# Kernel optimization log

Measured on AMD Instinct MI355X. Metric: run time of the kernel, lower is better.

The kernel has to match this reference:

```python
import jax, jax.numpy as jnp
import numpy as np

MODES, WIDTH, DEPTH, IN_F, OUT_F, HID = 8, 16, 3, 1, 1, 64


def setup_inputs() -> dict:
    key = jax.random.key(0)
    ks = jax.random.split(key, 12)
    B, H, W = 8, 512, 512
    scale = 1.0 / (WIDTH * WIDTH)
    inp = {
        'x': jax.random.normal(ks[0], (B, IN_F, H, W), dtype=jnp.float32),
        'fc0_w': jax.random.normal(ks[1], (IN_F, WIDTH), dtype=jnp.float32) * 0.5,
        'fc0_b': jax.random.normal(ks[2], (WIDTH,), dtype=jnp.float32) * 0.1,
        # complex spectral weights stored as real/imag parts, stacked over depth
        'spec_wr': jax.random.normal(ks[3], (DEPTH, WIDTH, WIDTH, MODES, MODES), dtype=jnp.float32) * scale,
        'spec_wi': jax.random.normal(ks[4], (DEPTH, WIDTH, WIDTH, MODES, MODES), dtype=jnp.float32) * scale,
        # 1x1 convs as [depth, out, in] matmuls + bias
        'conv_w': jax.random.normal(ks[5], (DEPTH, WIDTH, WIDTH), dtype=jnp.float32) * 0.25,
        'conv_b': jax.random.normal(ks[6], (DEPTH, WIDTH), dtype=jnp.float32) * 0.1,
        'fc1_w': jax.random.normal(ks[7], (WIDTH, HID), dtype=jnp.float32) * 0.25,
        'fc1_b': jax.random.normal(ks[8], (HID,), dtype=jnp.float32) * 0.1,
        'fc2_w': jax.random.normal(ks[9], (HID, OUT_F), dtype=jnp.float32) * 0.125,
        'fc2_b': jax.random.normal(ks[10], (OUT_F,), dtype=jnp.float32) * 0.1,
    }
    return inp


def _spectral_conv(x, w):
    # x: [B, Ci, H, W] real; w: [Ci, Co, m, m] complex
    B, C, H, W = x.shape
    m = w.shape[2]
    x_ft = jnp.fft.rfft2(x, norm='forward')  # [B, Ci, H, W//2+1]
    out_modes = jnp.einsum('bixy,ioxy->boxy', x_ft[:, :, :m, :m], w)
    out_ft = jnp.zeros((B, w.shape[1], H, W // 2 + 1), dtype=out_modes.dtype)
    out_ft = out_ft.at[:, :, :m, :m].set(out_modes)
    return jnp.fft.irfft2(out_ft, s=(H, W), norm='forward')


def reference(x, fc0_w, fc0_b, spec_wr, spec_wi, conv_w, conv_b, fc1_w, fc1_b, fc2_w, fc2_b):
    # lift: [B,C,H,W] -> channels-last linear -> [B,width,H,W]
    h = jnp.einsum('bchw,cd->bdhw', x, fc0_w) + fc0_b[None, :, None, None]
    for d in range(DEPTH):
        w_c = (spec_wr[d] + 1j * spec_wi[d]).astype(jnp.complex64)
        y = _spectral_conv(h, w_c)
        local = jnp.einsum('bchw,oc->bohw', h, conv_w[d]) + conv_b[d][None, :, None, None]
        h = y + local
    h = jnp.einsum('bchw,cd->bdhw', h, fc1_w) + fc1_b[None, :, None, None]
    h = jax.nn.relu(h)
    out = jnp.einsum('bchw,cd->bdhw', h, fc2_w) + fc2_b[None, :, None, None]
    return out
```

## Files before the change

### kernel.cpp

```cpp
#include <hip/hip_runtime.h>
#include <math.h>

#define NB 8
#define NH 512
#define NW 512
#define ANG512 0.01227184630308513f
#define SPEC_D 16384

#define DEV_SCOPE __HIP_MEMORY_SCOPE_AGENT

__global__ __launch_bounds__(256) void k_pre(const float* __restrict__ x,
                                             float* __restrict__ P,
                                             int* __restrict__ flags) {
    __shared__ float wred[8][16];
    const int tid = threadIdx.x;
    const int w = tid >> 6, lane = tid & 63;
    const int gid = blockIdx.x;
    const int b = gid >> 6, rg = gid & 63;

    if (gid == 0 && tid < 8)
        __hip_atomic_store(&flags[tid * 32], 0, __ATOMIC_RELAXED, DEV_SCOPE);

    #pragma unroll
    for (int rr = 0; rr < 2; ++rr) {
        const int row = rg * 8 + w + 4 * rr;
        const float* xr = x + ((size_t)(b * NH + row)) * NW;

        float p[16];
        #pragma unroll
        for (int j = 0; j < 16; ++j) p[j] = 0.f;

        #pragma unroll
        for (int j = 0; j < 4; ++j) {
            const int ww = lane + (j << 6);
            const float xa = xr[ww], xb = xr[ww + 256];
            const float a = xa + xb, d = xa - xb;
            float c1, s1;
            __sincosf(ANG512 * (float)ww, &s1, &c1);
            p[0] += a;
            p[1] = fmaf(d, c1, p[1]);
            p[9] = fmaf(-d, s1, p[9]);
            const float c2k = 2.f * c1;
            float ckm = 1.f, skm = 0.f, ck = c1, sk = s1;
            #pragma unroll
            for (int k = 2; k < 8; ++k) {
                const float cn = fmaf(c2k, ck, -ckm);
                const float sn = fmaf(c2k, sk, -skm);
                ckm = ck; skm = sk; ck = cn; sk = sn;
                const float v = (k & 1) ? d : a;
                p[k]     = fmaf(v, ck, p[k]);
                p[8 + k] = fmaf(-v, sk, p[8 + k]);
            }
        }
        #pragma unroll
        for (int m = 1; m < 64; m <<= 1) {
            #pragma unroll
            for (int j = 0; j < 16; ++j) p[j] += __shfl_xor(p[j], m);
        }
        if (lane < 16) wred[w + 4 * rr][lane] = p[lane];
    }
    __syncthreads();

    if (tid < 128) {
        const int kx = tid >> 4, q = tid & 15, qm = q & 7;
        float acc = 0.f;
        #pragma unroll
        for (int r = 0; r < 8; ++r) {
            const int row = rg * 8 + r;
            const int m = (kx * row) & 511;
            float cm, s2;
            __sincosf(ANG512 * (float)m, &s2, &cm);
            const float rre = wred[r][qm], rim = wred[r][8 + qm];
            acc += (q < 8) ? (rre * cm + rim * s2)
                           : (rim * cm - rre * s2);
        }
        P[((size_t)((b * 64 + rg) * 8 + kx)) * 16 + q] = acc;
    }
}

__device__ __forceinline__ void phaseC(
        const float* __restrict__ x, const float* __restrict__ AH,
        const float* __restrict__ gvec, const float* __restrict__ Kvec,
        const float* __restrict__ fc2_w, const float* __restrict__ fc2_b,
        float* __restrict__ out, float* sm) {
    float* WHr = sm;
    float* WHi = sm + 2048;

    const int tid = threadIdx.x;
    const int b = blockIdx.x >> 7;
    const int rp = blockIdx.x & 127;
    const int rl = tid >> 6;
    const int row = rp * 4 + rl;
    const int w0 = tid & 63;

    const float* xp = x + ((size_t)(b * NH + row)) * NW + w0;
    float xv[8];
    #pragma unroll
    for (int j = 0; j < 8; ++j) xv[j] = xp[j * 64];

    {
        float c1, s1;
        __sincosf(ANG512 * (float)row, &s1, &c1);
        float ctr[8], str[8];
        ctr[0] = 1.f; str[0] = 0.f; ctr[1] = c1; str[1] = s1;
        const float c2k = 2.f * c1;
        #pragma unroll
        for (int k = 2; k < 8; ++k) {
            ctr[k] = fmaf(c2k, ctr[k - 1], -ctr[k - 2]);
            str[k] = fmaf(c2k, str[k - 1], -str[k - 2]);
        }
        #pragma unroll
        for (int j = 0; j < 8; ++j) {
            const int idx = w0 + j * 64;
            const int hd = idx >> 3, ky = idx & 7;
            const float4* ap = (const float4*)(AH + ((size_t)(b * 64 + hd) * 8 + ky) * 16);
            const float4 a0 = ap[0], a1 = ap[1], a2 = ap[2], a3 = ap[3];
            float wr = a0.x, wi = a0.y;
            wr = fmaf(a0.z, ctr[1], wr); wr = fmaf(-a0.w, str[1], wr);
            wi = fmaf(a0.z, str[1], wi); wi = fmaf(a0.w, ctr[1], wi);
            wr = fmaf(a1.x, ctr[2], wr); wr = fmaf(-a1.y, str[2], wr);
            wi = fmaf(a1.x, str[2], wi); wi = fmaf(a1.y, ctr[2], wi);
            wr = fmaf(a1.z, ctr[3], wr); wr = fmaf(-a1.w, str[3], wr);
            wi = fmaf(a1.z, str[3], wi); wi = fmaf(a1.w, ctr[3], wi);
            wr = fmaf(a2.x, ctr[4], wr); wr = fmaf(-a2.y, str[4], wr);
            wi = fmaf(a2.x, str[4], wi); wi = fmaf(a2.y, ctr[4], wi);
            wr = fmaf(a2.z, ctr[5], wr); wr = fmaf(-a2.w, str[5], wr);
            wi = fmaf(a2.z, str[5], wi); wi = fmaf(a2.w, ctr[5], wi);
            wr = fmaf(a3.x, ctr[6], wr); wr = fmaf(-a3.y, str[6], wr);
            wi = fmaf(a3.x, str[6], wi); wi = fmaf(a3.y, ctr[6], wi);
            wr = fmaf(a3.z, ctr[7], wr); wr = fmaf(-a3.w, str[7], wr);
            wi = fmaf(a3.z, str[7], wi); wi = fmaf(a3.w, ctr[7], wi);
            if (ky == 0) wr += Kvec[hd];
            WHr[rl * 512 + idx] = wr;
            WHi[rl * 512 + idx] = wi;
        }
    }
    __syncthreads();

    {
        float c1, s1;
        __sincosf(ANG512 * (float)w0, &s1, &c1);
        float ct[8], st[8];
        ct[0] = 1.f; st[0] = 0.f; ct[1] = c1; st[1] = s1;
        const float c2k = 2.f * c1;
        #pragma unroll
        for (int k = 2; k < 8; ++k) {
            ct[k] = fmaf(c2k, ct[k - 1], -ct[k - 2]);
            st[k] = fmaf(c2k, st[k - 1], -st[k - 2]);
        }
        const float r2c = 0.70710678118654752f;
        const float* WR = WHr + rl * 512;
        const float* WI = WHi + rl * 512;
        const float fc2b = fc2_b[0];
        float acc[8];
        #pragma unroll
        for (int j = 0; j < 8; ++j) acc[j] = fc2b;

        #pragma unroll 4
        for (int hd = 0; hd < 64; ++hd) {
            const float4* r4 = (const float4*)(WR + hd * 8);
            const float4 wa = r4[0], wb = r4[1];
            const float4* i4 = (const float4*)(WI + hd * 8);
            const float4 va = i4[0], vb = i4[1];
            const float tr0 = wa.x;
            const float tr1 = wa.y * ct[1] - va.y * st[1];
            const float ti1 = wa.y * st[1] + va.y * ct[1];
            const float tr2 = wa.z * ct[2] - va.z * st[2];
            const float ti2 = wa.z * st[2] + va.z * ct[2];
            const float tr3 = wa.w * ct[3] - va.w * st[3];
            const float ti3 = wa.w * st[3] + va.w * ct[3];
            const float tr4 = wb.x * ct[4] - vb.x * st[4];
            const float tr5 = wb.y * ct[5] - vb.y * st[5];
            const float ti5 = wb.y * st[5] + vb.y * ct[5];
            const float tr6 = wb.z * ct[6] - vb.z * st[6];
            const float ti6 = wb.z * st[6] + vb.z * ct[6];
            const float tr7 = wb.w * ct[7] - vb.w * st[7];
            const float ti7 = wb.w * st[7] + vb.w * ct[7];

            const float gh = gvec[hd];
            const float w2 = fc2_w[hd];

            const float A0 = tr0 + tr4, A2 = tr2 + tr6;
            const float E = A0 + A2, D = A0 - A2;
            const float B13 = (tr1 + tr5) + (tr3 + tr7);
            const float U = (ti1 + ti5) - (ti3 + ti7);
            const float s0 = fmaf(gh, xv[0], E + B13);
            const float s2 = fmaf(gh, xv[2], D - U);
            const float s4 = fmaf(gh, xv[4], E - B13);
            const float s6 = fmaf(gh, xv[6], D + U);
            acc[0] = fmaf(fmaxf(s0, 0.f), w2, acc[0]);
            acc[2] = fmaf(fmaxf(s2, 0.f), w2, acc[2]);
            acc[4] = fmaf(fmaxf(s4, 0.f), w2, acc[4]);
            acc[6] = fmaf(fmaxf(s6, 0.f), w2, acc[6]);

            const float P = tr0 - tr4, Q = ti6 - ti2;
            const float E2 = P + Q, D2 = P - Q;
            const float B2 = r2c * (((tr1 - ti1) - (tr5 - ti5)) + ((tr7 + ti7) - (tr3 + ti3)));
            const float U2 = r2c * (((tr1 + ti1) - (tr5 + ti5)) - ((tr3 - ti3) + (ti7 - tr7)));
            const float s1p = fmaf(gh, xv[1], E2 + B2);
            const float s3p = fmaf(gh, xv[3], D2 - U2);
            const float s5p = fmaf(gh, xv[5], E2 - B2);
            const float s7p = fmaf(gh, xv[7], D2 + U2);
            acc[1] = fmaf(fmaxf(s1p, 0.f), w2, acc[1]);
            acc[3] = fmaf(fmaxf(s3p, 0.f), w2, acc[3]);
            acc[5] = fmaf(fmaxf(s5p, 0.f), w2, acc[5]);
            acc[7] = fmaf(fmaxf(s7p, 0.f), w2, acc[7]);
        }
        float* op = out + ((size_t)(b * NH + row)) * NW + w0;
        #pragma unroll
        for (int j = 0; j < 8; ++j) op[j * 64] = acc[j];
    }
}

__global__ __launch_bounds__(256, 4) void k_mh(
        const float* __restrict__ x, const float* __restrict__ P,
        const float* __restrict__ spec_wr, const float* __restrict__ spec_wi,
        const float* __restrict__ conv_w, const float* __restrict__ conv_b,
        const float* __restrict__ fc0_w, const float* __restrict__ fc0_b,
        const float* __restrict__ fc1_w, const float* __restrict__ fc1_b,
        const float* __restrict__ fc2_w, const float* __restrict__ fc2_b,
        float* __restrict__ AH, float* __restrict__ gv, float* __restrict__ Kv,
        int* __restrict__ flags, float* __restrict__ out) {
    __shared__ __align__(16) float sm[4096];
    const int tid = threadIdx.x;
    const int bid = blockIdx.x;

    if (bid < 64) {
        float* red2  = sm;
        float* X2    = sm + 256;
        float* Xr    = sm + 272;
        float* Xi    = sm + 400;
        float* Fr    = sm + 528;
        float* Fi    = sm + 656;
        float* Ar    = sm + 784;
        float* Ai    = sm + 912;
        float* Pm    = sm + 1040;
        float* fc1_s = sm + 1552;
        float* ps    = sm + 2576;

        const int b = bid >> 3;
        const int kx = bid & 7;

        {
            const int o = tid >> 4, c = tid & 15;
            float s = 0.f;
            for (int k = 0; k < 16; ++k)
                s += conv_w[512 + o * 16 + k] * conv_w[256 + k * 16 + c];
            Pm[tid] = s;
        }
        Pm[256 + tid] = conv_w[512 + tid];
        #pragma unroll
        for (int k = 0; k < 4; ++k) fc1_s[tid + k * 256] = fc1_w[tid + k * 256];

        {
            const int q = tid & 15, c = tid >> 4;
            float acc = 0.f;
            #pragma unroll
            for (int m = 0; m < 4; ++m) {
                const int rg = c + 16 * m;
                acc += P[((size_t)((b * 64 + rg) * 8 + kx)) * 16 + q];
            }
            red2[c * 16 + q] = acc;
        }
        __syncthreads();
        if (tid < 16) {
            float s = 0.f;
            #pragma unroll
            for (int c = 0; c < 16; ++c) s += red2[c * 16 + tid];
            X2[tid] = s;
        }
        __syncthreads();

        const bool act = (tid < 128);
        const int o = tid >> 3, ky = tid & 7;
        if (act) {
            const float inv = 1.f / (512.f * 512.f);
            float xr0 = fc0_w[o] * X2[ky] * inv;
            float xi0 = fc0_w[o] * X2[8 + ky] * inv;
            if (kx == 0 && ky == 0) xr0 += fc0_b[o];
            Xr[o * 8 + ky] = xr0; Xi[o * 8 + ky] = xi0;
            Ar[o * 8 + ky] = 0.f; Ai[o * 8 + ky] = 0.f;
        }
        __syncthreads();

        for (int dd = 0; dd < 3; ++dd) {
            if (act) {
                float fr = 0.f, fi = 0.f;
                const float* wrp = spec_wr + (size_t)dd * SPEC_D + o * 64 + kx * 8 + ky;
                const float* wip = spec_wi + (size_t)dd * SPEC_D + o * 64 + kx * 8 + ky;
                #pragma unroll
                for (int i = 0; i < 16; ++i) {
                    const float wre = wrp[i * 1024];
                    const float wim = wip[i * 1024];
                    const float xr0 = Xr[i * 8 + ky], xi0 = Xi[i * 8 + ky];
                    fr += xr0 * wre - xi0 * wim;
                    fi += xr0 * wim + xi0 * wre;
                }
                Fr[o * 8 + ky] = fr; Fi[o * 8 + ky] = fi;
            }
            __syncthreads();
            float xnr = 0.f, xni = 0.f;
            if (act) {
                float ar, ai;
                if (dd == 2) {
                    ar = Fr[o * 8 + ky]; ai = Fi[o * 8 + ky];
                } else {
                    ar = 0.f; ai = 0.f;
                    #pragma unroll
                    for (int c = 0; c < 16; ++c) {
                        const float pv = Pm[dd * 256 + o * 16 + c];
                        ar = fmaf(pv, Fr[c * 8 + ky], ar);
                        ai = fmaf(pv, Fi[c * 8 + ky], ai);
                    }
                }
                Ar[o * 8 + ky] += ar; Ai[o * 8 + ky] += ai;
                if (dd < 2) {
                    const float fr0 = Fr[o * 8 + ky], fi0 = Fi[o * 8 + ky];
                    if (ky == 0) {
                        if (kx == 0) { xnr = fr0; xni = 0.f; }
                        else         { xnr = 0.5f * fr0; xni = 0.5f * fi0; }
                    } else { xnr = fr0; xni = fi0; }
                    #pragma unroll
                    for (int c = 0; c < 16; ++c) {
                        const float cc = conv_w[dd * 256 + o * 16 + c];
                        xnr = fmaf(cc, Xr[c * 8 + ky], xnr);
                        xni = fmaf(cc, Xi[c * 8 + ky], xni);
                    }
                    if (kx == 0 && ky == 0) xnr += conv_b[dd * 16 + o];
                }
            }
            __syncthreads();
            if (act && dd < 2) { Xr[o * 8 + ky] = xnr; Xi[o * 8 + ky] = xni; }
            __syncthreads();
        }

        #pragma unroll
        for (int k2 = 0; k2 < 2; ++k2) {
            const int idx = tid + k2 * 256;
            const int hd = idx >> 3, ky2 = idx & 7;
            float ar = 0.f, ai = 0.f;
            #pragma unroll
            for (int c = 0; c < 16; ++c) {
                const float f = fc1_s[c * 64 + hd];
                ar = fmaf(f, Ar[c * 8 + ky2], ar);
                ai = fmaf(f, Ai[c * 8 + ky2], ai);
            }
            const float ck = (ky2 == 0) ? 1.f : 2.f;
            const size_t off = ((((size_t)(b * 64 + hd)) * 8 + ky2) * 8 + kx) * 2;
            __hip_atomic_store(&AH[off],     ck * ar, __ATOMIC_RELAXED, DEV_SCOPE);
            __hip_atomic_store(&AH[off + 1], ck * ai, __ATOMIC_RELAXED, DEV_SCOPE);
        }

        if (kx == 0) {
            if (tid < 16) {
                float su = 0.f, sb = 0.f;
                for (int c = 0; c < 16; ++c) {
                    su += conv_w[tid * 16 + c] * fc0_w[c];
                    sb += conv_w[tid * 16 + c] * fc0_b[c];
                }
                ps[tid] = su; ps[16 + tid] = sb;
            }
            __syncthreads();
            if (tid < 16) {
                float dv = 0.f, ev = conv_b[32 + tid];
                for (int k = 0; k < 16; ++k) {
                    dv += Pm[tid * 16 + k] * ps[k];
                    ev += Pm[tid * 16 + k] * (ps[16 + k] + conv_b[k]);
                    ev += conv_w[512 + tid * 16 + k] * conv_b[16 + k];
                }
                ps[32 + tid] = dv; ps[48 + tid] = ev;
            }
            __syncthreads();
            if (tid < 64) {
                float g = 0.f, K = fc1_b[tid];
                for (int c = 0; c < 16; ++c) {
                    g = fmaf(fc1_w[c * 64 + tid], ps[32 + c], g);
                    K = fmaf(fc1_w[c * 64 + tid], ps[48 + c], K);
                }
                __hip_atomic_store(&gv[b * 64 + tid], g, __ATOMIC_RELAXED, DEV_SCOPE);
                __hip_atomic_store(&Kv[b * 64 + tid], K, __ATOMIC_RELAXED, DEV_SCOPE);
            }
        }
        __syncthreads();
        if (tid == 0)
            __hip_atomic_fetch_add(&flags[b * 32], 1, __ATOMIC_RELEASE, DEV_SCOPE);
    }

    const int cb = bid >> 7;
    if (tid == 0) {
        while (__hip_atomic_load(&flags[cb * 32], __ATOMIC_RELAXED, DEV_SCOPE) < 8)
            __builtin_amdgcn_s_sleep(8);
    }
    __syncthreads();

    phaseC(x, AH, gv + cb * 64, Kv + cb * 64, fc2_w, fc2_b, out, sm);
}

extern "C" void kernel_launch(void* const* d_in, const int* in_sizes, int n_in,
                              void* d_out, int out_size, void* d_ws, size_t ws_size,
                              hipStream_t stream) {
    const float* x       = (const float*)d_in[0];
    const float* fc0_w   = (const float*)d_in[1];
    const float* fc0_b   = (const float*)d_in[2];
    const float* spec_wr = (const float*)d_in[3];
    const float* spec_wi = (const float*)d_in[4];
    const float* conv_w  = (const float*)d_in[5];
    const float* conv_b  = (const float*)d_in[6];
    const float* fc1_w   = (const float*)d_in[7];
    const float* fc1_b   = (const float*)d_in[8];
    const float* fc2_w   = (const float*)d_in[9];
    const float* fc2_b   = (const float*)d_in[10];
    float* outp = (float*)d_out;

    char* ws = (char*)d_ws;
    float* P   = (float*)ws;
    float* AH  = (float*)(ws + 262144);
    float* gv  = (float*)(ws + 524288);
    float* Kv  = (float*)(ws + 526336);
    int*  flg  = (int*)(ws + 528384);

    k_pre<<<512, 256, 0, stream>>>(x, P, flg);
    k_mh<<<1024, 256, 0, stream>>>(x, P, spec_wr, spec_wi, conv_w, conv_b,
                                   fc0_w, fc0_b, fc1_w, fc1_b, fc2_w, fc2_b,
                                   AH, gv, Kv, flg, outp);
}
```

Measured before the change: 143.8 us.

## Fuse pre-reduction kernel into main kernel with device-wide flag synchronization

Merges the separate pre-pass kernel into the main persistent kernel so that each of the 1024 blocks computes partial spectral projections for its own four rows. The partials are staged in the output buffer and published through global atomic counters. Per-batch blocks spin on these counters before reducing, and the counters are reset by the last consumer so no host-side reset is needed. This removes one kernel launch and the inter-kernel gap. In exchange it relies on all blocks being co-resident to avoid deadlock, and adds spin-wait latency plus extra atomic traffic.

```diff
diff --git a/kernel.cpp b/kernel.cpp
--- a/kernel.cpp
+++ b/kernel.cpp
@@ -9,27 +9,33 @@
 
 #define DEV_SCOPE __HIP_MEMORY_SCOPE_AGENT
 
-__global__ __launch_bounds__(256) void k_pre(const float* __restrict__ x,
-                                             float* __restrict__ P,
-                                             int* __restrict__ flags) {
-    __shared__ float wred[8][16];
+__device__ int g_pre[256];
+__device__ int g_flag[256];
+__device__ int g_done[256];
+
+__global__ __launch_bounds__(256, 4) void k_all(
+        const float* __restrict__ x,
+        const float* __restrict__ spec_wr, const float* __restrict__ spec_wi,
+        const float* __restrict__ conv_w, const float* __restrict__ conv_b,
+        const float* __restrict__ fc0_w, const float* __restrict__ fc0_b,
+        const float* __restrict__ fc1_w, const float* __restrict__ fc1_b,
+        const float* __restrict__ fc2_w, const float* __restrict__ fc2_b,
+        float* __restrict__ AH, float* __restrict__ gv, float* __restrict__ Kv,
+        float* out) {
+    __shared__ __align__(16) float sm[4096];
     const int tid = threadIdx.x;
-    const int w = tid >> 6, lane = tid & 63;
-    const int gid = blockIdx.x;
-    const int b = gid >> 6, rg = gid & 63;
-
-    if (gid == 0 && tid < 8)
-        __hip_atomic_store(&flags[tid * 32], 0, __ATOMIC_RELAXED, DEV_SCOPE);
-
-    #pragma unroll
-    for (int rr = 0; rr < 2; ++rr) {
-        const int row = rg * 8 + w + 4 * rr;
-        const float* xr = x + ((size_t)(b * NH + row)) * NW;
-
+    const int bid = blockIdx.x;
+    const int cb  = bid >> 7;
+    const int rp  = bid & 127;
+    const int rl  = tid >> 6;
+    const int lane = tid & 63;
+
+    {
+        const int row = rp * 4 + rl;
+        const float* xr = x + ((size_t)(cb * NH + row)) * NW;
         float p[16];
         #pragma unroll
         for (int j = 0; j < 16; ++j) p[j] = 0.f;
-
         #pragma unroll
         for (int j = 0; j < 4; ++j) {
             const int ww = lane + (j << 6);
@@ -57,173 +63,29 @@
             #pragma unroll
             for (int j = 0; j < 16; ++j) p[j] += __shfl_xor(p[j], m);
         }
-        if (lane < 16) wred[w + 4 * rr][lane] = p[lane];
+        if (lane < 16) sm[rl * 16 + lane] = p[lane];
     }
     __syncthreads();
-
     if (tid < 128) {
+        float* Pb = out + (size_t)cb * (NH * NW);
         const int kx = tid >> 4, q = tid & 15, qm = q & 7;
         float acc = 0.f;
         #pragma unroll
-        for (int r = 0; r < 8; ++r) {
-            const int row = rg * 8 + r;
-            const int m = (kx * row) & 511;
+        for (int r = 0; r < 4; ++r) {
+            const int rowr = rp * 4 + r;
+            const int m = (kx * rowr) & 511;
             float cm, s2;
             __sincosf(ANG512 * (float)m, &s2, &cm);
-            const float rre = wred[r][qm], rim = wred[r][8 + qm];
+            const float rre = sm[r * 16 + qm], rim = sm[r * 16 + 8 + qm];
             acc += (q < 8) ? (rre * cm + rim * s2)
                            : (rim * cm - rre * s2);
         }
-        P[((size_t)((b * 64 + rg) * 8 + kx)) * 16 + q] = acc;
-    }
-}
-
-__device__ __forceinline__ void phaseC(
-        const float* __restrict__ x, const float* __restrict__ AH,
-        const float* __restrict__ gvec, const float* __restrict__ Kvec,
-        const float* __restrict__ fc2_w, const float* __restrict__ fc2_b,
-        float* __restrict__ out, float* sm) {
-    float* WHr = sm;
-    float* WHi = sm + 2048;
-
-    const int tid = threadIdx.x;
-    const int b = blockIdx.x >> 7;
-    const int rp = blockIdx.x & 127;
-    const int rl = tid >> 6;
-    const int row = rp * 4 + rl;
-    const int w0 = tid & 63;
-
-    const float* xp = x + ((size_t)(b * NH + row)) * NW + w0;
-    float xv[8];
-    #pragma unroll
-    for (int j = 0; j < 8; ++j) xv[j] = xp[j * 64];
-
-    {
-        float c1, s1;
-        __sincosf(ANG512 * (float)row, &s1, &c1);
-        float ctr[8], str[8];
-        ctr[0] = 1.f; str[0] = 0.f; ctr[1] = c1; str[1] = s1;
-        const float c2k = 2.f * c1;
-        #pragma unroll
-        for (int k = 2; k < 8; ++k) {
-            ctr[k] = fmaf(c2k, ctr[k - 1], -ctr[k - 2]);
-            str[k] = fmaf(c2k, str[k - 1], -str[k - 2]);
-        }
-        #pragma unroll
-        for (int j = 0; j < 8; ++j) {
-            const int idx = w0 + j * 64;
-            const int hd = idx >> 3, ky = idx & 7;
-            const float4* ap = (const float4*)(AH + ((size_t)(b * 64 + hd) * 8 + ky) * 16);
-            const float4 a0 = ap[0], a1 = ap[1], a2 = ap[2], a3 = ap[3];
-            float wr = a0.x, wi = a0.y;
-            wr = fmaf(a0.z, ctr[1], wr); wr = fmaf(-a0.w, str[1], wr);
-            wi = fmaf(a0.z, str[1], wi); wi = fmaf(a0.w, ctr[1], wi);
-            wr = fmaf(a1.x, ctr[2], wr); wr = fmaf(-a1.y, str[2], wr);
-            wi = fmaf(a1.x, str[2], wi); wi = fmaf(a1.y, ctr[2], wi);
-            wr = fmaf(a1.z, ctr[3], wr); wr = fmaf(-a1.w, str[3], wr);
-            wi = fmaf(a1.z, str[3], wi); wi = fmaf(a1.w, ctr[3], wi);
-            wr = fmaf(a2.x, ctr[4], wr); wr = fmaf(-a2.y, str[4], wr);
-            wi = fmaf(a2.x, str[4], wi); wi = fmaf(a2.y, ctr[4], wi);
-            wr = fmaf(a2.z, ctr[5], wr); wr = fmaf(-a2.w, str[5], wr);
-            wi = fmaf(a2.z, str[5], wi); wi = fmaf(a2.w, ctr[5], wi);
-            wr = fmaf(a3.x, ctr[6], wr); wr = fmaf(-a3.y, str[6], wr);
-            wi = fmaf(a3.x, str[6], wi); wi = fmaf(a3.y, ctr[6], wi);
-            wr = fmaf(a3.z, ctr[7], wr); wr = fmaf(-a3.w, str[7], wr);
-            wi = fmaf(a3.z, str[7], wi); wi = fmaf(a3.w, ctr[7], wi);
-            if (ky == 0) wr += Kvec[hd];
-            WHr[rl * 512 + idx] = wr;
-            WHi[rl * 512 + idx] = wi;
-        }
+        __hip_atomic_store(&Pb[((rp << 3) + kx) * 16 + q],
+                           acc, __ATOMIC_RELAXED, DEV_SCOPE);
     }
     __syncthreads();
-
-    {
-        float c1, s1;
-        __sincosf(ANG512 * (float)w0, &s1, &c1);
-        float ct[8], st[8];
-        ct[0] = 1.f; st[0] = 0.f; ct[1] = c1; st[1] = s1;
-        const float c2k = 2.f * c1;
-        #pragma unroll
-        for (int k = 2; k < 8; ++k) {
-            ct[k] = fmaf(c2k, ct[k - 1], -ct[k - 2]);
-            st[k] = fmaf(c2k, st[k - 1], -st[k - 2]);
-        }
-        const float r2c = 0.70710678118654752f;
-        const float* WR = WHr + rl * 512;
-        const float* WI = WHi + rl * 512;
-        const float fc2b = fc2_b[0];
-        float acc[8];
-        #pragma unroll
-        for (int j = 0; j < 8; ++j) acc[j] = fc2b;
-
-        #pragma unroll 4
-        for (int hd = 0; hd < 64; ++hd) {
-            const float4* r4 = (const float4*)(WR + hd * 8);
-            const float4 wa = r4[0], wb = r4[1];
-            const float4* i4 = (const float4*)(WI + hd * 8);
-            const float4 va = i4[0], vb = i4[1];
-            const float tr0 = wa.x;
-            const float tr1 = wa.y * ct[1] - va.y * st[1];
-            const float ti1 = wa.y * st[1] + va.y * ct[1];
-            const float tr2 = wa.z * ct[2] - va.z * st[2];
-            const float ti2 = wa.z * st[2] + va.z * ct[2];
-            const float tr3 = wa.w * ct[3] - va.w * st[3];
-            const float ti3 = wa.w * st[3] + va.w * ct[3];
-            const float tr4 = wb.x * ct[4] - vb.x * st[4];
-            const float tr5 = wb.y * ct[5] - vb.y * st[5];
-            const float ti5 = wb.y * st[5] + vb.y * ct[5];
-            const float tr6 = wb.z * ct[6] - vb.z * st[6];
-            const float ti6 = wb.z * st[6] + vb.z * ct[6];
-            const float tr7 = wb.w * ct[7] - vb.w * st[7];
-            const float ti7 = wb.w * st[7] + vb.w * ct[7];
-
-            const float gh = gvec[hd];
-            const float w2 = fc2_w[hd];
-
-            const float A0 = tr0 + tr4, A2 = tr2 + tr6;
-            const float E = A0 + A2, D = A0 - A2;
-            const float B13 = (tr1 + tr5) + (tr3 + tr7);
-            const float U = (ti1 + ti5) - (ti3 + ti7);
-            const float s0 = fmaf(gh, xv[0], E + B13);
-            const float s2 = fmaf(gh, xv[2], D - U);
-            const float s4 = fmaf(gh, xv[4], E - B13);
-            const float s6 = fmaf(gh, xv[6], D + U);
-            acc[0] = fmaf(fmaxf(s0, 0.f), w2, acc[0]);
-            acc[2] = fmaf(fmaxf(s2, 0.f), w2, acc[2]);
-            acc[4] = fmaf(fmaxf(s4, 0.f), w2, acc[4]);
-            acc[6] = fmaf(fmaxf(s6, 0.f), w2, acc[6]);
-
-            const float P = tr0 - tr4, Q = ti6 - ti2;
-            const float E2 = P + Q, D2 = P - Q;
-            const float B2 = r2c * (((tr1 - ti1) - (tr5 - ti5)) + ((tr7 + ti7) - (tr3 + ti3)));
-            const float U2 = r2c * (((tr1 + ti1) - (tr5 + ti5)) - ((tr3 - ti3) + (ti7 - tr7)));
-            const float s1p = fmaf(gh, xv[1], E2 + B2);
-            const float s3p = fmaf(gh, xv[3], D2 - U2);
-            const float s5p = fmaf(gh, xv[5], E2 - B2);
-            const float s7p = fmaf(gh, xv[7], D2 + U2);
-            acc[1] = fmaf(fmaxf(s1p, 0.f), w2, acc[1]);
-            acc[3] = fmaf(fmaxf(s3p, 0.f), w2, acc[3]);
-            acc[5] = fmaf(fmaxf(s5p, 0.f), w2, acc[5]);
-            acc[7] = fmaf(fmaxf(s7p, 0.f), w2, acc[7]);
-        }
-        float* op = out + ((size_t)(b * NH + row)) * NW + w0;
-        #pragma unroll
-        for (int j = 0; j < 8; ++j) op[j * 64] = acc[j];
-    }
-}
-
-__global__ __launch_bounds__(256, 4) void k_mh(
-        const float* __restrict__ x, const float* __restrict__ P,
-        const float* __restrict__ spec_wr, const float* __restrict__ spec_wi,
-        const float* __restrict__ conv_w, const float* __restrict__ conv_b,
-        const float* __restrict__ fc0_w, const float* __restrict__ fc0_b,
-        const float* __restrict__ fc1_w, const float* __restrict__ fc1_b,
-        const float* __restrict__ fc2_w, const float* __restrict__ fc2_b,
-        float* __restrict__ AH, float* __restrict__ gv, float* __restrict__ Kv,
-        int* __restrict__ flags, float* __restrict__ out) {
-    __shared__ __align__(16) float sm[4096];
-    const int tid = threadIdx.x;
-    const int bid = blockIdx.x;
+    if (tid == 0)
+        __hip_atomic_fetch_add(&g_pre[cb * 32], 1, __ATOMIC_RELEASE, DEV_SCOPE);
 
     if (bid < 64) {
         float* red2  = sm;
@@ -252,15 +114,22 @@
         #pragma unroll
         for (int k = 0; k < 4; ++k) fc1_s[tid + k * 256] = fc1_w[tid + k * 256];
 
+        if (tid == 0) {
+            while (__hip_atomic_load(&g_pre[b * 32], __ATOMIC_RELAXED, DEV_SCOPE) < 128)
+                __builtin_amdgcn_s_sleep(2);
+        }
+        __syncthreads();
+
         {
-            const int q = tid & 15, c = tid >> 4;
+            const float* Pb = out + (size_t)b * (NH * NW);
+            const int q = tid & 15, gg = tid >> 4;
             float acc = 0.f;
             #pragma unroll
-            for (int m = 0; m < 4; ++m) {
-                const int rg = c + 16 * m;
-                acc += P[((size_t)((b * 64 + rg) * 8 + kx)) * 16 + q];
-            }
-            red2[c * 16 + q] = acc;
+            for (int m = 0; m < 8; ++m) {
+                const int g = gg + 16 * m;
+                acc += Pb[((g << 3) + kx) * 16 + q];
+            }
+            red2[gg * 16 + q] = acc;
         }
         __syncthreads();
         if (tid < 16) {
@@ -383,17 +252,149 @@
         }
         __syncthreads();
         if (tid == 0)
-            __hip_atomic_fetch_add(&flags[b * 32], 1, __ATOMIC_RELEASE, DEV_SCOPE);
+            __hip_atomic_fetch_add(&g_flag[b * 32], 1, __ATOMIC_RELEASE, DEV_SCOPE);
     }
 
-    const int cb = bid >> 7;
     if (tid == 0) {
-        while (__hip_atomic_load(&flags[cb * 32], __ATOMIC_RELAXED, DEV_SCOPE) < 8)
+        while (__hip_atomic_load(&g_flag[cb * 32], __ATOMIC_RELAXED, DEV_SCOPE) < 8)
             __builtin_amdgcn_s_sleep(8);
+        const int d = __hip_atomic_fetch_add(&g_done[cb * 32], 1,
+                                             __ATOMIC_RELAXED, DEV_SCOPE);
+        if (d == 127) {
+            __hip_atomic_store(&g_flag[cb * 32], 0, __ATOMIC_RELAXED, DEV_SCOPE);
+            __hip_atomic_store(&g_done[cb * 32], 0, __ATOMIC_RELAXED, DEV_SCOPE);
+            __hip_atomic_store(&g_pre[cb * 32],  0, __ATOMIC_RELAXED, DEV_SCOPE);
+        }
     }
     __syncthreads();
 
-    phaseC(x, AH, gv + cb * 64, Kv + cb * 64, fc2_w, fc2_b, out, sm);
+    {
+        float* WHr = sm;
+        float* WHi = sm + 2048;
+        const int b = cb;
+        const int row = rp * 4 + rl;
+        const int w0 = tid & 63;
+        const float* gvec = gv + cb * 64;
+        const float* Kvec = Kv + cb * 64;
+
+        const float* xp = x + ((size_t)(b * NH + row)) * NW + w0;
+        float xv[8];
+        #pragma unroll
+        for (int j = 0; j < 8; ++j) xv[j] = xp[j * 64];
+
+        {
+            float c1, s1;
+            __sincosf(ANG512 * (float)row, &s1, &c1);
+            float ctr[8], str[8];
+            ctr[0] = 1.f; str[0] = 0.f; ctr[1] = c1; str[1] = s1;
+            const float c2k = 2.f * c1;
+            #pragma unroll
+            for (int k = 2; k < 8; ++k) {
+                ctr[k] = fmaf(c2k, ctr[k - 1], -ctr[k - 2]);
+                str[k] = fmaf(c2k, str[k - 1], -str[k - 2]);
+            }
+            #pragma unroll
+            for (int j = 0; j < 8; ++j) {
+                const int idx = w0 + j * 64;
+                const int hd = idx >> 3, ky = idx & 7;
+                const float4* ap = (const float4*)(AH + ((size_t)(b * 64 + hd) * 8 + ky) * 16);
+                const float4 a0 = ap[0], a1 = ap[1], a2 = ap[2], a3 = ap[3];
+                float wr = a0.x, wi = a0.y;
+                wr = fmaf(a0.z, ctr[1], wr); wr = fmaf(-a0.w, str[1], wr);
+                wi = fmaf(a0.z, str[1], wi); wi = fmaf(a0.w, ctr[1], wi);
+                wr = fmaf(a1.x, ctr[2], wr); wr = fmaf(-a1.y, str[2], wr);
+                wi = fmaf(a1.x, str[2], wi); wi = fmaf(a1.y, ctr[2], wi);
+                wr = fmaf(a1.z, ctr[3], wr); wr = fmaf(-a1.w, str[3], wr);
+                wi = fmaf(a1.z, str[3], wi); wi = fmaf(a1.w, ctr[3], wi);
+                wr = fmaf(a2.x, ctr[4], wr); wr = fmaf(-a2.y, str[4], wr);
+                wi = fmaf(a2.x, str[4], wi); wi = fmaf(a2.y, ctr[4], wi);
+                wr = fmaf(a2.z, ctr[5], wr); wr = fmaf(-a2.w, str[5], wr);
+                wi = fmaf(a2.z, str[5], wi); wi = fmaf(a2.w, ctr[5], wi);
+                wr = fmaf(a3.x, ctr[6], wr); wr = fmaf(-a3.y, str[6], wr);
+                wi = fmaf(a3.x, str[6], wi); wi = fmaf(a3.y, ctr[6], wi);
+                wr = fmaf(a3.z, ctr[7], wr); wr = fmaf(-a3.w, str[7], wr);
+                wi = fmaf(a3.z, str[7], wi); wi = fmaf(a3.w, ctr[7], wi);
+                if (ky == 0) wr += Kvec[hd];
+                WHr[rl * 512 + idx] = wr;
+                WHi[rl * 512 + idx] = wi;
+            }
+        }
+        __syncthreads();
+
+        {
+            float c1, s1;
+            __sincosf(ANG512 * (float)w0, &s1, &c1);
+            float ct[8], st[8];
+            ct[0] = 1.f; st[0] = 0.f; ct[1] = c1; st[1] = s1;
+            const float c2k = 2.f * c1;
+            #pragma unroll
+            for (int k = 2; k < 8; ++k) {
+                ct[k] = fmaf(c2k, ct[k - 1], -ct[k - 2]);
+                st[k] = fmaf(c2k, st[k - 1], -st[k - 2]);
+            }
+            const float r2c = 0.70710678118654752f;
+            const float* WR = WHr + rl * 512;
+            const float* WI = WHi + rl * 512;
+            const float fc2b = fc2_b[0];
+            float acc[8];
+            #pragma unroll
+            for (int j = 0; j < 8; ++j) acc[j] = fc2b;
+
+            #pragma unroll 4
+            for (int hd = 0; hd < 64; ++hd) {
+                const float4* r4 = (const float4*)(WR + hd * 8);
+                const float4 wa = r4[0], wb = r4[1];
+                const float4* i4 = (const float4*)(WI + hd * 8);
+                const float4 va = i4[0], vb = i4[1];
+                const float tr0 = wa.x;
+                const float tr1 = wa.y * ct[1] - va.y * st[1];
+                const float ti1 = wa.y * st[1] + va.y * ct[1];
+                const float tr2 = wa.z * ct[2] - va.z * st[2];
+                const float ti2 = wa.z * st[2] + va.z * ct[2];
+                const float tr3 = wa.w * ct[3] - va.w * st[3];
+                const float ti3 = wa.w * st[3] + va.w * ct[3];
+                const float tr4 = wb.x * ct[4] - vb.x * st[4];
+                const float tr5 = wb.y * ct[5] - vb.y * st[5];
+                const float ti5 = wb.y * st[5] + vb.y * ct[5];
+                const float tr6 = wb.z * ct[6] - vb.z * st[6];
+                const float ti6 = wb.z * st[6] + vb.z * ct[6];
+                const float tr7 = wb.w * ct[7] - vb.w * st[7];
+                const float ti7 = wb.w * st[7] + vb.w * ct[7];
+
+                const float gh = gvec[hd];
+                const float w2 = fc2_w[hd];
+
+                const float A0 = tr0 + tr4, A2 = tr2 + tr6;
+                const float E = A0 + A2, D = A0 - A2;
+                const float B13 = (tr1 + tr5) + (tr3 + tr7);
+                const float U = (ti1 + ti5) - (ti3 + ti7);
+                const float s0 = fmaf(gh, xv[0], E + B13);
+                const float s2 = fmaf(gh, xv[2], D - U);
+                const float s4 = fmaf(gh, xv[4], E - B13);
+                const float s6 = fmaf(gh, xv[6], D + U);
+                acc[0] = fmaf(fmaxf(s0, 0.f), w2, acc[0]);
+                acc[2] = fmaf(fmaxf(s2, 0.f), w2, acc[2]);
+                acc[4] = fmaf(fmaxf(s4, 0.f), w2, acc[4]);
+                acc[6] = fmaf(fmaxf(s6, 0.f), w2, acc[6]);
+
+                const float Pq = tr0 - tr4, Q = ti6 - ti2;
+                const float E2 = Pq + Q, D2 = Pq - Q;
+                const float B2 = r2c * (((tr1 - ti1) - (tr5 - ti5)) + ((tr7 + ti7) - (tr3 + ti3)));
+                const float U2 = r2c * (((tr1 + ti1) - (tr5 + ti5)) - ((tr3 - ti3) + (ti7 - tr7)));
+                const float s1p = fmaf(gh, xv[1], E2 + B2);
+                const float s3p = fmaf(gh, xv[3], D2 - U2);
+                const float s5p = fmaf(gh, xv[5], E2 - B2);
+                const float s7p = fmaf(gh, xv[7], D2 + U2);
+                acc[1] = fmaf(fmaxf(s1p, 0.f), w2, acc[1]);
+                acc[3] = fmaf(fmaxf(s3p, 0.f), w2, acc[3]);
+                acc[5] = fmaf(fmaxf(s5p, 0.f), w2, acc[5]);
+                acc[7] = fmaf(fmaxf(s7p, 0.f), w2, acc[7]);
+            }
+            float* op = out + ((size_t)(b * NH + row)) * NW + w0;
+            #pragma unroll
+            for (int j = 0; j < 8; ++j) op[j * 64] = acc[j];
+        }
+    }
 }
 
 extern "C" void kernel_launch(void* const* d_in, const int* in_sizes, int n_in,
@@ -413,14 +414,11 @@
     float* outp = (float*)d_out;
 
     char* ws = (char*)d_ws;
-    float* P   = (float*)ws;
-    float* AH  = (float*)(ws + 262144);
-    float* gv  = (float*)(ws + 524288);
-    float* Kv  = (float*)(ws + 526336);
-    int*  flg  = (int*)(ws + 528384);
-
-    k_pre<<<512, 256, 0, stream>>>(x, P, flg);
-    k_mh<<<1024, 256, 0, stream>>>(x, P, spec_wr, spec_wi, conv_w, conv_b,
-                                   fc0_w, fc0_b, fc1_w, fc1_b, fc2_w, fc2_b,
-                                   AH, gv, Kv, flg, outp);
+    float* AH = (float*)ws;
+    float* gv = (float*)(ws + 262144);
+    float* Kv = (float*)(ws + 264192);
+
+    k_all<<<1024, 256, 0, stream>>>(x, spec_wr, spec_wi, conv_w, conv_b,
+                                    fc0_w, fc0_b, fc1_w, fc1_b, fc2_w, fc2_b,
+                                    AH, gv, Kv, outp);
 }
```

Measured after the change: 158.0 us. 1.1x slower.
